# Kernel optimization log

Hardware: AMD Instinct MI355X
Metric: run time of the kernel (lower is better)

The kernel has to match this reference:

```python
import jax, jax.numpy as jnp
import numpy as np

B, H, W, C = 4, 64, 64, 64


def conv1x1(x, w, b):
    # 1x1 conv on channels_last input == per-pixel dense layer
    return jnp.einsum('bhwc,cd->bhwd', x, w) + b


def setup_inputs() -> dict:
    key = jax.random.key(0)
    ks = jax.random.split(key, 8)
    std = 1.0 / np.sqrt(C)
    inp = {
        'x': jax.random.normal(ks[0], (B, H, W, C), dtype=jnp.float32),
        'wq_s': jax.random.normal(ks[1], (C, C), dtype=jnp.float32) * std,
        'bq_s': jnp.zeros((C,), jnp.float32),
        'wk_s': jax.random.normal(ks[2], (C, C), dtype=jnp.float32) * std,
        'bk_s': jnp.zeros((C,), jnp.float32),
        'wv_s': jax.random.normal(ks[3], (C, C), dtype=jnp.float32) * std,
        'bv_s': jnp.zeros((C,), jnp.float32),
        'wq_c': jax.random.normal(ks[4], (C, C), dtype=jnp.float32) * std,
        'bq_c': jnp.zeros((C,), jnp.float32),
        'wk_c': jax.random.normal(ks[5], (C, C), dtype=jnp.float32) * std,
        'bk_c': jnp.zeros((C,), jnp.float32),
        'wv_c': jax.random.normal(ks[6], (C, C), dtype=jnp.float32) * std,
        'bv_c': jnp.zeros((C,), jnp.float32),
        'a': jnp.float32(0.0),
        'b': jnp.float32(0.0),
    }
    return inp


def reference(x, wq_s, bq_s, wk_s, bk_s, wv_s, bv_s,
              wq_c, bq_c, wk_c, bk_c, wv_c, bv_c, a, b):
    scale = jnp.sqrt(jnp.float32(C))
    N = H * W

    # ---- Spatial self-attention: tokens = pixels, (B, HW, C) ----
    qs = conv1x1(x, wq_s, bq_s).reshape(B, N, C)
    ks_ = conv1x1(x, wk_s, bk_s).reshape(B, N, C)
    vs = conv1x1(x, wv_s, bv_s).reshape(B, N, C)
    att_s = jax.nn.softmax(jnp.einsum('bnc,bmc->bnm', qs, ks_) / scale, axis=-1)
    spat = jnp.einsum('bnm,bmc->bnc', att_s, vs).reshape(B, H, W, C)

    # ---- Channel self-attention ----
    # Faithful to the TF code: raw reshape of channels_last (B,H,W,C) -> (B,C,HW)
    # (a memory reinterpretation, NOT a transpose).
    qc = conv1x1(x, wq_c, bq_c).reshape(B, C, N)
    kc = conv1x1(x, wk_c, bk_c).reshape(B, C, N)
    vc = conv1x1(x, wv_c, bv_c).reshape(B, C, N)
    att_c = jax.nn.softmax(jnp.einsum('bcn,bdn->bcd', qc, kc) / scale, axis=-1)
    chan = jnp.einsum('bcd,bdn->bcn', att_c, vc).reshape(B, H, W, C)

    # ---- Scaled residual fusion ----
    return (b * spat + x) + (a * chan + x)
```

## Files before the change

kernel.cpp:

```cpp
#include <hip/hip_runtime.h>

#define NTOK 4096
#define PSTR 72

typedef short bf16x8 __attribute__((ext_vector_type(8)));
typedef short bf16x4 __attribute__((ext_vector_type(4)));
typedef float f32x4 __attribute__((ext_vector_type(4)));

__device__ __forceinline__ short f2bf(float f) {
  union { float f; unsigned u; } v; v.f = f;
  unsigned r = v.u + 0x7fffu + ((v.u >> 16) & 1u);
  return (short)(r >> 16);
}
__device__ __forceinline__ short f2bf_t(float f) {
  union { float f; unsigned u; } v; v.f = f;
  return (short)(v.u >> 16);
}
__device__ __forceinline__ float bf2f(short s) {
  union { unsigned u; float f; } v; v.u = ((unsigned)(unsigned short)s) << 16;
  return v.f;
}

struct PrepArgs {
  const float* w[6];
  short* wt;
};

struct ConvArgs {
  const float* x;
  const short* wt;
  const float* bias[6];
  short* out[6];
};

#define QSC (0.125f * 1.44269504088896f)

__global__ __launch_bounds__(256) void prep_w(PrepArgs p) {
  const int wi = blockIdx.x;
  const float* w = p.w[wi];
  short* o = p.wt + wi*4096;
  const int d = threadIdx.x & 63, cb = (threadIdx.x >> 6) * 16;
  const float sc = (wi == 0 || wi == 3) ? QSC : 1.f;
  bf16x8 v0, v1;
  for (int j=0;j<8;j++) {
    v0[j] = f2bf(w[(cb+j)*64 + d] * sc);
    v1[j] = f2bf(w[(cb+8+j)*64 + d] * sc);
  }
  *(bf16x8*)(o + d*64 + cb)     = v0;
  *(bf16x8*)(o + d*64 + cb + 8) = v1;
}

__global__ __launch_bounds__(256) void conv_qkv(ConvArgs args) {
  __shared__ __align__(16) short lT[64*PSTR];
  const int tid = threadIdx.x;
  const int wave = tid >> 6, lane = tid & 63;
  const int quad = lane >> 4, l16 = lane & 15;
  const int half = blockIdx.y;

  int row = blockIdx.x * 64 + wave*16 + l16;
  const float* xr = args.x + (size_t)row*64 + quad*8;
  f32x4 x0 = *(const f32x4*)xr;
  f32x4 x1 = *(const f32x4*)(xr+4);
  f32x4 x2 = *(const f32x4*)(xr+32);
  f32x4 x3 = *(const f32x4*)(xr+36);
  bf16x8 a0, a1;
  for (int j=0;j<4;j++){ a0[j]=f2bf(x0[j]); a0[4+j]=f2bf(x1[j]); a1[j]=f2bf(x2[j]); a1[4+j]=f2bf(x3[j]); }

  int orow_base = blockIdx.x*64 + wave*16 + quad*4;
  for (int j=0; j<3; j++) {
    const int wi = half*3 + j;
    const short* wtp = args.wt + wi*4096;
    for (int dt=0; dt<4; dt++) {
      bf16x8 b0 = *(const bf16x8*)(wtp + (dt*16+l16)*64 + quad*8);
      bf16x8 b1 = *(const bf16x8*)(wtp + (dt*16+l16)*64 + 32 + quad*8);
      f32x4 acc = {0.f,0.f,0.f,0.f};
      acc = __builtin_amdgcn_mfma_f32_16x16x32_bf16(a0, b0, acc, 0,0,0);
      acc = __builtin_amdgcn_mfma_f32_16x16x32_bf16(a1, b1, acc, 0,0,0);
      float bias = args.bias[wi][dt*16+l16];
      if (wi == 0 || wi == 3) bias *= QSC;
      if (wi != 2) {
        short* outp = args.out[wi];
        for (int r=0;r<4;r++)
          outp[(size_t)(orow_base + r)*64 + dt*16 + l16] = f2bf(acc[r] + bias);
      } else {
        for (int r=0;r<4;r++)
          lT[(dt*16+l16)*PSTR + wave*16 + quad*4 + r] = f2bf(acc[r] + bias);
      }
    }
  }
  if (half == 0) {
    __syncthreads();
    int b  = (blockIdx.x*64) >> 12;
    int n0 = (blockIdx.x*64) & 4095;
    for (int u0=0; u0<2; u0++) {
      int u = u0*256 + tid;
      int c = u >> 3, t8 = u & 7;
      *(bf16x8*)(args.out[2] + (size_t)(b*64+c)*4096 + n0 + t8*8) =
          *(const bf16x8*)&lT[c*PSTR + t8*8];
    }
  }
}

__global__ __launch_bounds__(256, 3) void attn_part(const short* __restrict__ qs,
    const short* __restrict__ ks, const short* __restrict__ vst,
    short* __restrict__ opart, float* __restrict__ ml) {
  __shared__ __align__(16) short sK[2][64*PSTR];
  __shared__ __align__(16) short sV[2][64*PSTR];
  __shared__ __align__(16) short sP[4][16*PSTR];
  const int tid = threadIdx.x;
  const int wave = tid>>6, lane = tid&63, quad = lane>>4, l16 = lane&15;
  const int qtile = blockIdx.x*2 + (wave>>1);
  const int qgo = (wave&1)*2;
  const int batch = blockIdx.y, kg = blockIdx.z;
  const int srow = tid >> 3, sc8 = tid & 7;
  const int ntile  = (kg < 4) ? 11 : 10;
  const int k0base = ((kg < 4) ? kg*11 : 44 + (kg-4)*10) * 64;

  const short* kb  = ks  + (size_t)batch*NTOK*64;
  const short* vtb = vst + (size_t)batch*64*NTOK;

  bf16x8 qa[2][2];
  for (int qg=0;qg<2;qg++) {
    const short* qp = qs + ((size_t)batch*NTOK + qtile*64 + (qgo+qg)*16 + l16)*64;
    qa[qg][0] = *(const bf16x8*)(qp + quad*8);
    qa[qg][1] = *(const bf16x8*)(qp + 32 + quad*8);
  }

  f32x4 ot[2][4];
  for (int qg=0;qg<2;qg++) for (int ct=0;ct<4;ct++) ot[qg][ct]=(f32x4){0.f,0.f,0.f,0.f};
  float lq[2] = {0.f,0.f};

  for (int h=0;h<2;h++) {
    int row = (h*256+tid)>>3, c8 = (h*256+tid)&7;
    *(bf16x8*)&sK[0][row*PSTR + c8*8] = *(const bf16x8*)(kb + (size_t)(k0base+row)*64 + c8*8);
    *(bf16x8*)&sV[0][row*PSTR + c8*8] = *(const bf16x8*)(vtb + (size_t)row*4096 + k0base + c8*8);
  }
  __syncthreads();

  for (int t=0; t<ntile; t++) {
    const int cur = t & 1;
    bf16x8 gk0, gk1, gv0, gv1;
    const bool pf = (t+1 < ntile);
    if (pf) {
      int k0 = k0base + (t+1)*64;
      gk0 = *(const bf16x8*)(kb + (size_t)(k0+srow)*64 + sc8*8);
      gv0 = *(const bf16x8*)(vtb + (size_t)srow*4096 + k0 + sc8*8);
      gk1 = *(const bf16x8*)(kb + (size_t)(k0+32+srow)*64 + sc8*8);
      gv1 = *(const bf16x8*)(vtb + (size_t)(32+srow)*4096 + k0 + sc8*8);
    }

    bf16x8 kf[4][2], vf[4][2];
    for (int mt=0;mt<4;mt++) {
      kf[mt][0] = *(const bf16x8*)&sK[cur][(mt*16+l16)*PSTR + quad*8];
      kf[mt][1] = *(const bf16x8*)&sK[cur][(mt*16+l16)*PSTR + 32 + quad*8];
      vf[mt][0] = *(const bf16x8*)&sV[cur][(mt*16+l16)*PSTR + quad*8];
      vf[mt][1] = *(const bf16x8*)&sV[cur][(mt*16+l16)*PSTR + 32 + quad*8];
    }

    for (int qg=0;qg<2;qg++) {
      f32x4 st[4];
      for (int mt=0;mt<4;mt++) {
        f32x4 z = {0.f,0.f,0.f,0.f};
        z = __builtin_amdgcn_mfma_f32_16x16x32_bf16(kf[mt][0], qa[qg][0], z, 0,0,0);
        z = __builtin_amdgcn_mfma_f32_16x16x32_bf16(kf[mt][1], qa[qg][1], z, 0,0,0);
        st[mt] = z;
      }
      float sum = 0.f;
      for (int mt=0;mt<4;mt++)
        for (int r=0;r<4;r++) {
          float p = __builtin_amdgcn_exp2f(st[mt][r]);
          st[mt][r] = p; sum += p;
        }
      lq[qg] += sum;
      short* lPw = sP[wave];
      for (int mt=0;mt<4;mt++) {
        bf16x4 pk;
        for (int r=0;r<4;r++) pk[r] = f2bf_t(st[mt][r]);
        *(bf16x4*)&lPw[l16*PSTR + mt*16 + quad*4] = pk;
      }
      bf16x8 pb0 = *(const bf16x8*)&lPw[l16*PSTR + quad*8];
      bf16x8 pb1 = *(const bf16x8*)&lPw[l16*PSTR + 32 + quad*8];
      for (int ct=0;ct<4;ct++) {
        ot[qg][ct] = __builtin_amdgcn_mfma_f32_16x16x32_bf16(vf[ct][0], pb0, ot[qg][ct], 0,0,0);
        ot[qg][ct] = __builtin_amdgcn_mfma_f32_16x16x32_bf16(vf[ct][1], pb1, ot[qg][ct], 0,0,0);
      }
    }

    if (pf) {
      int nxt = cur ^ 1;
      *(bf16x8*)&sK[nxt][srow*PSTR + sc8*8]      = gk0;
      *(bf16x8*)&sV[nxt][srow*PSTR + sc8*8]      = gv0;
      *(bf16x8*)&sK[nxt][(32+srow)*PSTR + sc8*8] = gk1;
      *(bf16x8*)&sV[nxt][(32+srow)*PSTR + sc8*8] = gv1;
    }
    __syncthreads();
  }

  size_t obase = (((size_t)batch*64 + qtile)*6 + kg) * 4096;
  for (int qg=0;qg<2;qg++)
    for (int ct=0;ct<4;ct++) {
      bf16x4 pk;
      for (int r=0;r<4;r++) pk[r] = f2bf(ot[qg][ct][r]);
      *(bf16x4*)&opart[obase + (size_t)((qgo+qg)*1024 + ct*256 + quad*64 + l16*4)] = pk;
    }
  float lt[2];
  for (int qg=0;qg<2;qg++) {
    float s = lq[qg];
    s += __shfl_xor(s, 16);
    s += __shfl_xor(s, 32);
    lt[qg] = s;
  }
  if (quad == 0) {
    float* mlp = ml + (((size_t)batch*64 + qtile)*6 + kg)*64;
    for (int qg=0;qg<2;qg++)
      mlp[(qgo+qg)*16 + l16] = lt[qg];
  }
}

__global__ __launch_bounds__(256) void chan_qk_part(const short* __restrict__ qc,
    const short* __restrict__ kc, float* __restrict__ Gpart) {
  const int tid = threadIdx.x;
  const int wave = tid>>6, lane = tid&63, quad = lane>>4, l16 = lane&15;
  const int ks_ = blockIdx.x, b = blockIdx.y;
  const int n0 = ks_*64;
  const short* qb = qc + (size_t)b*NTOK*64;
  const short* kb = kc + (size_t)b*NTOK*64;

  bf16x8 aq0 = *(const bf16x8*)(qb + (size_t)(wave*16+l16)*4096 + n0 + quad*8);
  bf16x8 aq1 = *(const bf16x8*)(qb + (size_t)(wave*16+l16)*4096 + n0 + 32 + quad*8);
  f32x4 acc[4];
  for (int nt=0;nt<4;nt++) {
    bf16x8 bk0 = *(const bf16x8*)(kb + (size_t)(nt*16+l16)*4096 + n0 + quad*8);
    bf16x8 bk1 = *(const bf16x8*)(kb + (size_t)(nt*16+l16)*4096 + n0 + 32 + quad*8);
    f32x4 z = {0.f,0.f,0.f,0.f};
    z = __builtin_amdgcn_mfma_f32_16x16x32_bf16(aq0, bk0, z, 0,0,0);
    z = __builtin_amdgcn_mfma_f32_16x16x32_bf16(aq1, bk1, z, 0,0,0);
    acc[nt] = z;
  }
  float* gp = Gpart + ((size_t)b*64 + ks_)*4096;
  for (int nt=0;nt<4;nt++)
    for (int r=0;r<4;r++)
      gp[(wave*16 + quad*4 + r)*64 + nt*16 + l16] = acc[nt][r];
}

__global__ __launch_bounds__(256) void combine_fuse(const short* __restrict__ opart,
    const float* __restrict__ ml, const float* __restrict__ Gpart,
    const short* __restrict__ vc, const float* __restrict__ x,
    const float* __restrict__ pa, const float* __restrict__ pb,
    float* __restrict__ out) {
  __shared__ float sInv[64];
  __shared__ float sAtt[64];
  const int qt = blockIdx.x, b = blockIdx.y, hz = blockIdx.z, t = threadIdx.x;
  const size_t base6 = ((size_t)b*64 + qt)*6;
  if (t < 64) {
    float den = 0.f;
    for (int kg=0;kg<6;kg++) den += ml[(base6+kg)*64 + t];
    sInv[t] = 1.f/den;
    float g = 0.f;
    const float* gp = Gpart + (size_t)b*64*4096 + qt*64 + t;
    for (int ks=0; ks<64; ks++) g += gp[(size_t)ks*4096];
    float m = g;
    for (int off=1; off<64; off<<=1) m = fmaxf(m, __shfl_xor(m, off));
    float p = __builtin_amdgcn_exp2f(g - m);
    float s = p;
    for (int off=1; off<64; off<<=1) s += __shfl_xor(s, off);
    sAtt[t] = p/s;
  }
  __syncthreads();

  const int e0 = hz*2048 + t*8;
  const int q = e0 >> 6;
  const int qg = q >> 4, l16 = q & 15;
  const int seg = (t&7) >> 1, quad0 = (t&1)*2;

  float accS[8];
  for (int j=0;j<8;j++) accS[j]=0.f;
  for (int kg=0;kg<6;kg++) {
    const short* op = opart + (base6+kg)*4096 + qg*1024 + seg*256 + l16*4;
    bf16x4 c0 = *(const bf16x4*)(op + quad0*64);
    bf16x4 c1 = *(const bf16x4*)(op + (quad0+1)*64);
    for (int r=0;r<4;r++) { accS[r] += bf2f(c0[r]); accS[4+r] += bf2f(c1[r]); }
  }
  float inv = sInv[q];
  float accC[8];
  for (int j=0;j<8;j++) accC[j]=0.f;
  const short* vb = vc + (size_t)b*NTOK*64;
  for (int d=0; d<64; d++) {
    bf16x8 v = *(const bf16x8*)(vb + (size_t)d*4096 + e0);
    float a = sAtt[d];
    for (int j=0;j<8;j++) accC[j] += a*bf2f(v[j]);
  }
  const float av = pa[0], bv = pb[0];
  size_t flat = ((size_t)b*64 + qt)*4096 + e0;
  f32x4 x0 = *(const f32x4*)(x + flat);
  f32x4 x1 = *(const f32x4*)(x + flat + 4);
  f32x4 r0, r1;
  for (int j=0;j<4;j++) {
    r0[j] = bv*accS[j]*inv   + av*accC[j]   + 2.f*x0[j];
    r1[j] = bv*accS[4+j]*inv + av*accC[4+j] + 2.f*x1[j];
  }
  *(f32x4*)(out + flat)     = r0;
  *(f32x4*)(out + flat + 4) = r1;
}

extern "C" void kernel_launch(void* const* d_in, const int* in_sizes, int n_in,
                              void* d_out, int out_size, void* d_ws, size_t ws_size,
                              hipStream_t stream) {
  const float* x = (const float*)d_in[0];
  char* ws = (char*)d_ws;
  const size_t MB = 1048576;
  short* qs    = (short*)(ws + 0*MB);
  short* ks_   = (short*)(ws + 2*MB);
  short* vst   = (short*)(ws + 4*MB);
  short* qc    = (short*)(ws + 6*MB);
  short* kc    = (short*)(ws + 8*MB);
  short* vc    = (short*)(ws + 10*MB);
  short* opart = (short*)(ws + 12*MB);
  float* ml    = (float*)(ws + 24*MB);
  short* wt    = (short*)(ws + 25*MB);
  float* Gpart = (float*)(ws + 0*MB);

  PrepArgs pa;
  ConvArgs ca;
  ca.x = x; ca.wt = wt;
  for (int i=0;i<6;i++) {
    pa.w[i]    = (const float*)d_in[1+2*i];
    ca.bias[i] = (const float*)d_in[2+2*i];
  }
  pa.wt = wt;
  ca.out[0]=qs; ca.out[1]=ks_; ca.out[2]=vst;
  ca.out[3]=qc; ca.out[4]=kc; ca.out[5]=vc;

  hipLaunchKernelGGL(prep_w, dim3(6), dim3(256), 0, stream, pa);
  hipLaunchKernelGGL(conv_qkv, dim3(256,2), dim3(256), 0, stream, ca);
  hipLaunchKernelGGL(attn_part, dim3(32,4,6), dim3(256), 0, stream, qs, ks_, vst, opart, ml);
  hipLaunchKernelGGL(chan_qk_part, dim3(64,4), dim3(256), 0, stream, qc, kc, Gpart);
  hipLaunchKernelGGL(combine_fuse, dim3(64,4,2), dim3(256), 0, stream,
                     opart, ml, Gpart, vc, x, (const float*)d_in[13], (const float*)d_in[14],
                     (float*)d_out);
}
```

Measured before the change: 140.7 us.

## Split channel attention into reduce-softmax and MFMA AV kernels

Moves the channel-attention Gpart reduction and softmax out of combine_fuse into a dedicated kernel, so it is done once per batch instead of once per query tile. The att·V product is computed with bf16 MFMA in a new kernel that stages V transposed in LDS, writing a bf16 chan buffer. combine_fuse then only reads the precomputed result. This adds two kernel launches, an extra round trip through global memory for chan, and rounds att and chan to bf16.

Measured after the change: 144.4 us. 1.03x slower.

```diff
diff --git a/kernel.cpp b/kernel.cpp
--- a/kernel.cpp
+++ b/kernel.cpp
@@ -243,28 +243,80 @@
       gp[(wave*16 + quad*4 + r)*64 + nt*16 + l16] = acc[nt][r];
 }
 
+__global__ __launch_bounds__(256) void chan_reduce_sm(const float* __restrict__ Gpart,
+    float* __restrict__ att) {
+  const int cg = blockIdx.x, b = blockIdx.y, t = threadIdx.x;
+  const int c = cg*16 + (t>>4), dq = t & 15;
+  const float* gp = Gpart + (size_t)b*64*4096 + c*64 + dq*4;
+  f32x4 acc = {0.f,0.f,0.f,0.f};
+  for (int ks_=0; ks_<64; ks_++)
+    acc += *(const f32x4*)(gp + (size_t)ks_*4096);
+  float mx = fmaxf(fmaxf(acc[0],acc[1]), fmaxf(acc[2],acc[3]));
+  mx = fmaxf(mx, __shfl_xor(mx, 1));
+  mx = fmaxf(mx, __shfl_xor(mx, 2));
+  mx = fmaxf(mx, __shfl_xor(mx, 4));
+  mx = fmaxf(mx, __shfl_xor(mx, 8));
+  f32x4 p; float sum = 0.f;
+  for (int j=0;j<4;j++){ p[j] = __builtin_amdgcn_exp2f(acc[j]-mx); sum += p[j]; }
+  sum += __shfl_xor(sum, 1);
+  sum += __shfl_xor(sum, 2);
+  sum += __shfl_xor(sum, 4);
+  sum += __shfl_xor(sum, 8);
+  float inv = 1.f/sum;
+  f32x4 r; for (int j=0;j<4;j++) r[j] = p[j]*inv;
+  *(f32x4*)(att + (size_t)b*4096 + c*64 + dq*4) = r;
+}
+
+__global__ __launch_bounds__(256) void chan_av_mfma(const float* __restrict__ att,
+    const short* __restrict__ vc, short* __restrict__ chan) {
+  __shared__ __align__(16) short sVt[128*72];
+  const int tid = threadIdx.x;
+  const int wave = tid>>6, lane = tid&63, quad = lane>>4, l16 = lane&15;
+  const int b = blockIdx.y, n0 = blockIdx.x*128;
+  const short* vb = vc + (size_t)b*NTOK*64;
+
+  for (int it=0; it<4; it++) {
+    int d = it*16 + (tid>>4);
+    int nl8 = (tid&15)*8;
+    bf16x8 gv = *(const bf16x8*)(vb + (size_t)d*4096 + n0 + nl8);
+    for (int j=0;j<8;j++) sVt[(nl8+j)*72 + d] = gv[j];
+  }
+  const float* ab = att + (size_t)b*4096;
+  bf16x8 aq[4][2];
+  for (int mt=0;mt<4;mt++)
+    for (int kh=0;kh<2;kh++) {
+      const float* ap = ab + (mt*16+l16)*64 + kh*32 + quad*8;
+      f32x4 a0 = *(const f32x4*)ap, a1 = *(const f32x4*)(ap+4);
+      for (int j=0;j<4;j++){ aq[mt][kh][j]=f2bf(a0[j]); aq[mt][kh][4+j]=f2bf(a1[j]); }
+    }
+  __syncthreads();
+
+  short* cb = chan + (size_t)b*262144;
+  for (int nt=0;nt<2;nt++) {
+    int nl = wave*32 + nt*16 + l16;
+    bf16x8 bv0 = *(const bf16x8*)&sVt[nl*72 + quad*8];
+    bf16x8 bv1 = *(const bf16x8*)&sVt[nl*72 + 32 + quad*8];
+    for (int mt=0;mt<4;mt++) {
+      f32x4 acc = {0.f,0.f,0.f,0.f};
+      acc = __builtin_amdgcn_mfma_f32_16x16x32_bf16(aq[mt][0], bv0, acc, 0,0,0);
+      acc = __builtin_amdgcn_mfma_f32_16x16x32_bf16(aq[mt][1], bv1, acc, 0,0,0);
+      for (int r=0;r<4;r++)
+        cb[(size_t)(mt*16+quad*4+r)*4096 + n0 + nl] = f2bf(acc[r]);
+    }
+  }
+}
+
 __global__ __launch_bounds__(256) void combine_fuse(const short* __restrict__ opart,
-    const float* __restrict__ ml, const float* __restrict__ Gpart,
-    const short* __restrict__ vc, const float* __restrict__ x,
-    const float* __restrict__ pa, const float* __restrict__ pb,
-    float* __restrict__ out) {
+    const float* __restrict__ ml, const short* __restrict__ chan,
+    const float* __restrict__ x, const float* __restrict__ pa,
+    const float* __restrict__ pb, float* __restrict__ out) {
   __shared__ float sInv[64];
-  __shared__ float sAtt[64];
   const int qt = blockIdx.x, b = blockIdx.y, hz = blockIdx.z, t = threadIdx.x;
   const size_t base6 = ((size_t)b*64 + qt)*6;
   if (t < 64) {
     float den = 0.f;
     for (int kg=0;kg<6;kg++) den += ml[(base6+kg)*64 + t];
     sInv[t] = 1.f/den;
-    float g = 0.f;
-    const float* gp = Gpart + (size_t)b*64*4096 + qt*64 + t;
-    for (int ks=0; ks<64; ks++) g += gp[(size_t)ks*4096];
-    float m = g;
-    for (int off=1; off<64; off<<=1) m = fmaxf(m, __shfl_xor(m, off));
-    float p = __builtin_amdgcn_exp2f(g - m);
-    float s = p;
-    for (int off=1; off<64; off<<=1) s += __shfl_xor(s, off);
-    sAtt[t] = p/s;
   }
   __syncthreads();
 
@@ -282,22 +334,15 @@
     for (int r=0;r<4;r++) { accS[r] += bf2f(c0[r]); accS[4+r] += bf2f(c1[r]); }
   }
   float inv = sInv[q];
-  float accC[8];
-  for (int j=0;j<8;j++) accC[j]=0.f;
-  const short* vb = vc + (size_t)b*NTOK*64;
-  for (int d=0; d<64; d++) {
-    bf16x8 v = *(const bf16x8*)(vb + (size_t)d*4096 + e0);
-    float a = sAtt[d];
-    for (int j=0;j<8;j++) accC[j] += a*bf2f(v[j]);
-  }
+  bf16x8 cv = *(const bf16x8*)(chan + (size_t)b*262144 + qt*4096 + e0);
   const float av = pa[0], bv = pb[0];
   size_t flat = ((size_t)b*64 + qt)*4096 + e0;
   f32x4 x0 = *(const f32x4*)(x + flat);
   f32x4 x1 = *(const f32x4*)(x + flat + 4);
   f32x4 r0, r1;
   for (int j=0;j<4;j++) {
-    r0[j] = bv*accS[j]*inv   + av*accC[j]   + 2.f*x0[j];
-    r1[j] = bv*accS[4+j]*inv + av*accC[4+j] + 2.f*x1[j];
+    r0[j] = bv*accS[j]*inv   + av*bf2f(cv[j])   + 2.f*x0[j];
+    r1[j] = bv*accS[4+j]*inv + av*bf2f(cv[4+j]) + 2.f*x1[j];
   }
   *(f32x4*)(out + flat)     = r0;
   *(f32x4*)(out + flat + 4) = r1;
@@ -318,6 +363,8 @@
   short* opart = (short*)(ws + 12*MB);
   float* ml    = (float*)(ws + 24*MB);
   short* wt    = (short*)(ws + 25*MB);
+  float* att   = (float*)(ws + 25*MB + 524288);
+  short* chan  = (short*)(ws + 26*MB);
   float* Gpart = (float*)(ws + 0*MB);
 
   PrepArgs pa;
@@ -335,7 +382,9 @@
   hipLaunchKernelGGL(conv_qkv, dim3(256,2), dim3(256), 0, stream, ca);
   hipLaunchKernelGGL(attn_part, dim3(32,4,6), dim3(256), 0, stream, qs, ks_, vst, opart, ml);
   hipLaunchKernelGGL(chan_qk_part, dim3(64,4), dim3(256), 0, stream, qc, kc, Gpart);
+  hipLaunchKernelGGL(chan_reduce_sm, dim3(4,4), dim3(256), 0, stream, Gpart, att);
+  hipLaunchKernelGGL(chan_av_mfma, dim3(32,4), dim3(256), 0, stream, att, vc, chan);
   hipLaunchKernelGGL(combine_fuse, dim3(64,4,2), dim3(256), 0, stream,
-                     opart, ml, Gpart, vc, x, (const float*)d_in[13], (const float*)d_in[14],
+                     opart, ml, chan, x, (const float*)d_in[13], (const float*)d_in[14],
                      (float*)d_out);
 }
```
